# Kernel tuning notes

Hardware: AMD Instinct MI355X
Metric: run time of the kernel (lower is better)

The kernel has to match this reference:

```python
import jax, jax.numpy as jnp
import numpy as np
from jax import lax

B, IMG, P, CIN = 8, 224, 16, 3
D, NH, E, HID, DEPTH, NC = 768, 12, 4, 3072, 12, 1000
NPAT = (IMG // P) ** 2  # 196
S = NPAT + 1            # 197 tokens incl cls
HD = D // NH            # 64
EPS = 1e-5


def _ln(x, g, b):
    m = jnp.mean(x, axis=-1, keepdims=True)
    v = jnp.mean((x - m) ** 2, axis=-1, keepdims=True)
    return (x - m) * lax.rsqrt(v + EPS) * g + b


def setup_inputs() -> dict:
    key = jax.random.key(0)
    ks = list(jax.random.split(key, 24))
    def rn(k, shape, s=0.02):
        return (jax.random.normal(k, shape) * s).astype(jnp.float32)
    inp = {
        "x": jax.random.normal(ks[0], (B, CIN, IMG, IMG), dtype=jnp.float32),
        "patch_w": rn(ks[1], (D, CIN, P, P)),
        "patch_b": jnp.zeros((D,), jnp.float32),
        "cls_token": jnp.zeros((1, 1, D), jnp.float32),
        "pos_embed": rn(ks[2], (1, S, D)),
        "ln1_g": jnp.ones((DEPTH, D), jnp.float32),
        "ln1_b": jnp.zeros((DEPTH, D), jnp.float32),
        "ln2_g": jnp.ones((DEPTH, D), jnp.float32),
        "ln2_b": jnp.zeros((DEPTH, D), jnp.float32),
        "attn_in_w": rn(ks[3], (DEPTH, 3 * D, D)),
        "attn_in_b": jnp.zeros((DEPTH, 3 * D), jnp.float32),
        "attn_out_w": rn(ks[4], (DEPTH, D, D)),
        "attn_out_b": jnp.zeros((DEPTH, D), jnp.float32),
        "gate_w": rn(ks[5], (DEPTH, E, D)),
        "gate_b": jnp.zeros((DEPTH, E), jnp.float32),
        "w1": rn(ks[6], (DEPTH, E, D, HID)),
        "b1": jnp.zeros((DEPTH, E, HID), jnp.float32),
        "w2": rn(ks[7], (DEPTH, E, HID, D)),
        "b2": jnp.zeros((DEPTH, E, D), jnp.float32),
        "head_w": rn(ks[8], (NC, D)),
        "head_b": jnp.zeros((NC,), jnp.float32),
    }
    return inp


def _forward(x, patch_w, patch_b, cls_token, pos_embed, ln1_g, ln1_b, ln2_g, ln2_b,
             attn_in_w, attn_in_b, attn_out_w, attn_out_b, gate_w, gate_b,
             w1, b1, w2, b2, head_w, head_b):
    # Patch embedding: conv stride=patch, then flatten spatial -> tokens
    feat = lax.conv_general_dilated(x, patch_w, window_strides=(P, P), padding="VALID",
                                    dimension_numbers=("NCHW", "OIHW", "NCHW"))
    t = feat.reshape(B, D, NPAT).transpose(0, 2, 1) + patch_b  # [B, 196, D]
    cls = jnp.broadcast_to(cls_token, (B, 1, D))
    h = jnp.concatenate([cls, t], axis=1) + pos_embed  # [B, S, D]

    scale = 1.0 / np.sqrt(HD).astype(np.float32)
    for i in range(DEPTH):
        # ---- attention (query = LN(x); key/value = x, as in source) ----
        qn = _ln(h, ln1_g[i], ln1_b[i])
        wq, wk, wv = attn_in_w[i, :D], attn_in_w[i, D:2 * D], attn_in_w[i, 2 * D:]
        bq, bk, bv = attn_in_b[i, :D], attn_in_b[i, D:2 * D], attn_in_b[i, 2 * D:]
        q = (qn @ wq.T + bq).reshape(B, S, NH, HD)
        k = (h @ wk.T + bk).reshape(B, S, NH, HD)
        v = (h @ wv.T + bv).reshape(B, S, NH, HD)
        scores = jnp.einsum("bqhd,bkhd->bhqk", q, k) * scale
        attn = jax.nn.softmax(scores, axis=-1)
        o = jnp.einsum("bhqk,bkhd->bqhd", attn, v).reshape(B, S, D)
        h = h + o @ attn_out_w[i].T + attn_out_b[i]

        # ---- Top-1 gated MoE MLP ----
        y = _ln(h, ln2_g[i], ln2_b[i])
        logits = y @ gate_w[i].T + gate_b[i]            # [B,S,E]
        probs = jax.nn.softmax(logits, axis=-1)
        top = jnp.argmax(probs, axis=-1)                # [B,S]
        onehot = jax.nn.one_hot(top, E, dtype=y.dtype)  # [B,S,E]
        gv = jnp.sum(probs * onehot, axis=-1)           # [B,S] top-1 gate score
        hidd = jax.nn.gelu(jnp.einsum("bsd,edh->besh", y, w1[i]) + b1[i][None, :, None, :])
        eout = jnp.einsum("besh,ehd->besd", hidd, w2[i]) + b2[i][None, :, None, :]
        moe = jnp.einsum("bse,besd->bsd", onehot, eout) * gv[..., None]
        h = h + moe

    return h[:, 0] @ head_w.T + head_b  # [B, NC]


def reference(x, patch_w, patch_b, cls_token, pos_embed, ln1_g, ln1_b, ln2_g, ln2_b,
              attn_in_w, attn_in_b, attn_out_w, attn_out_b, gate_w, gate_b,
              w1, b1, w2, b2, head_w, head_b):
    return _forward(x, patch_w, patch_b, cls_token, pos_embed, ln1_g, ln1_b, ln2_g,
                    ln2_b, attn_in_w, attn_in_b, attn_out_w, attn_out_b, gate_w,
                    gate_b, w1, b1, w2, b2, head_w, head_b)
```

## Files before the change

### kernel.cpp

```cpp
#include <hip/hip_runtime.h>
#include <math.h>


#define BB 8
#define SS 197
#define DD 768
#define MT (BB*SS)
#define NPATCH 196
#define MPE (BB*NPATCH)
#define HHID 3072
#define NEXP 4
#define QKVN 2304

typedef __bf16 bf16_t;
typedef bf16_t bf16x8 __attribute__((ext_vector_type(8)));
typedef float  f32x4  __attribute__((ext_vector_type(4)));

__device__ __forceinline__ void gload16(const bf16_t* g, bf16_t* l) {
    __builtin_amdgcn_global_load_lds(
        (const __attribute__((address_space(1))) unsigned int*)g,
        (__attribute__((address_space(3))) unsigned int*)l,
        16, 0, 0);
}

__device__ __forceinline__ bf16x8 cvt8(float4 a, float4 b) {
    bf16x8 o;
    o[0]=(bf16_t)a.x; o[1]=(bf16_t)a.y; o[2]=(bf16_t)a.z; o[3]=(bf16_t)a.w;
    o[4]=(bf16_t)b.x; o[5]=(bf16_t)b.y; o[6]=(bf16_t)b.z; o[7]=(bf16_t)b.w;
    return o;
}

__global__ void gather_patches(const float* __restrict__ x, bf16_t* __restrict__ Xp) {
    int i = blockIdx.x * 256 + threadIdx.x;
    if (i >= MPE * DD) return;
    int k = i % DD;
    int m = i / DD;
    int pw = k & 15, ph = (k >> 4) & 15, cin = k >> 8;
    int px = m % 14, py = (m / 14) % 14, b = m / NPATCH;
    int row = py * 16 + ph, col = px * 16 + pw;
    Xp[i] = (bf16_t)x[((size_t)(b * 3 + cin) * 224 + row) * 224 + col];
}

__global__ void build_h(const float* __restrict__ pe, const float* __restrict__ patch_b,
                        const float* __restrict__ cls, const float* __restrict__ pos,
                        float* __restrict__ h) {
    int i = blockIdx.x * 256 + threadIdx.x;
    if (i >= MT * DD) return;
    int d = i % DD;
    int s = (i / DD) % SS;
    int b = i / (DD * SS);
    float v;
    if (s == 0) v = cls[d];
    else        v = pe[((size_t)(b * NPATCH) + (s - 1)) * DD + d] + patch_b[d];
    h[i] = v + pos[s * DD + d];
}

__global__ void cvt_bf16(const float* __restrict__ in, bf16_t* __restrict__ out, int n) {
    int i = (blockIdx.x * 256 + threadIdx.x) * 8;
    if (i >= n) return;
    const float4* p = (const float4*)(in + i);
    *(bf16x8*)(out + i) = cvt8(p[0], p[1]);
}

__global__ __launch_bounds__(256) void transpose_cvt(const float* __restrict__ in,
                                                     bf16_t* __restrict__ out, int R, int C) {
    int z = blockIdx.z;
    in  += (size_t)z * R * C;
    out += (size_t)z * R * C;
    __shared__ float t[32][33];
    int c0 = blockIdx.x * 32, r0 = blockIdx.y * 32;
    int tx = threadIdx.x & 31, ty = threadIdx.x >> 5;
    #pragma unroll
    for (int i = 0; i < 4; i++)
        t[ty + 8*i][tx] = in[(size_t)(r0 + ty + 8*i) * C + c0 + tx];
    __syncthreads();
    #pragma unroll
    for (int i = 0; i < 4; i++)
        out[(size_t)(c0 + ty + 8*i) * R + r0 + tx] = (bf16_t)t[tx][ty + 8*i];
}

template<int BM, int BN, int WM, int WN, int MODE>
__global__ __launch_bounds__((BM/WM)*(BN/WN)*64) void gemm_bf16(
    const bf16_t* __restrict__ A, const bf16_t* __restrict__ A2, int nsplit,
    const bf16_t* __restrict__ Bw,
    const float* __restrict__ bias, float* __restrict__ C, bf16_t* __restrict__ Cb,
    const int* __restrict__ cnt, const int* __restrict__ idx,
    const float* __restrict__ gv, int M, int N, int K)
{
    constexpr int NW  = (BM/WM)*(BN/WN);
    constexpr int WNC = BN/WN;
    constexpr int MI  = WM/16;
    constexpr int NI  = WN/16;
    constexpr int IA  = (BM/8)/NW;
    constexpr int IB  = (BN/8)/NW;
    constexpr bool GATHER = (MODE == 3 || MODE == 4);

    int z = blockIdx.z;
    int count = GATHER ? cnt[z] : M;
    int m0 = blockIdx.y * BM;
    if (m0 >= count) return;
    int n0 = blockIdx.x * BN;
    if (n0 >= nsplit) A = A2;
    Bw += (size_t)z * N * K;
    const float* biasz = bias ? (bias + (size_t)z * N) : nullptr;

    __shared__ bf16_t As[2][BM * 64];
    __shared__ bf16_t Bs[2][BN * 64];
    __shared__ int toks[BM];

    int tid = threadIdx.x, lane = tid & 63, w = tid >> 6;
    if (tid < BM) {
        int mm = m0 + tid;
        if (mm > count - 1) mm = count - 1;
        toks[tid] = GATHER ? idx[z * MT + mm] : mm;
    }
    __syncthreads();

    int wm = (w / WNC) * WM, wn = (w % WNC) * WN;
    int fr = lane & 15, fs = lane >> 4;

    f32x4 acc[MI][NI];
    #pragma unroll
    for (int mi = 0; mi < MI; mi++)
        #pragma unroll
        for (int ni = 0; ni < NI; ni++)
            #pragma unroll
            for (int j = 0; j < 4; j++) acc[mi][ni][j] = 0.f;

    int nk = K >> 6;
    int srow = lane >> 3, scc = lane & 7;

    #define STAGE(buf, k0)                                                              \
        {                                                                               \
            _Pragma("unroll")                                                           \
            for (int i = 0; i < IA; i++) {                                              \
                int blk = i*NW + w;                                                     \
                int row = blk*8 + srow;                                                 \
                const bf16_t* s = A + (size_t)toks[row] * K + (k0) + ((scc ^ (row & 7)) << 3); \
                gload16(s, &As[buf][blk * 512]);                                        \
            }                                                                           \
            _Pragma("unroll")                                                           \
            for (int i = 0; i < IB; i++) {                                              \
                int blk = i*NW + w;                                                     \
                int row = blk*8 + srow;                                                 \
                const bf16_t* s = Bw + (size_t)(n0 + row) * K + (k0) + ((scc ^ (row & 7)) << 3); \
                gload16(s, &Bs[buf][blk * 512]);                                        \
            }                                                                           \
        }

    STAGE(0, 0);
    __syncthreads();
    int cur = 0;
    for (int t = 0; t < nk; t++) {
        if (t + 1 < nk) STAGE(cur ^ 1, (t + 1) << 6);
        #pragma unroll
        for (int ks = 0; ks < 2; ks++) {
            bf16x8 af[MI], bfr[NI];
            #pragma unroll
            for (int mi = 0; mi < MI; mi++) {
                int r = wm + mi * 16 + fr;
                af[mi] = *(bf16x8*)&As[cur][r * 64 + (((fs + ks*4) ^ (r & 7)) << 3)];
            }
            #pragma unroll
            for (int ni = 0; ni < NI; ni++) {
                int r = wn + ni * 16 + fr;
                bfr[ni] = *(bf16x8*)&Bs[cur][r * 64 + (((fs + ks*4) ^ (r & 7)) << 3)];
            }
            #pragma unroll
            for (int mi = 0; mi < MI; mi++)
                #pragma unroll
                for (int ni = 0; ni < NI; ni++)
                    acc[mi][ni] = __builtin_amdgcn_mfma_f32_16x16x32_bf16(af[mi], bfr[ni], acc[mi][ni], 0, 0, 0);
        }
        __syncthreads();
        cur ^= 1;
    }
    #undef STAGE

    #pragma unroll
    for (int mi = 0; mi < MI; mi++) {
        #pragma unroll
        for (int j = 0; j < 4; j++) {
            int rr = wm + mi * 16 + fs * 4 + j;
            if (m0 + rr >= count) continue;
            int crow = toks[rr];
            #pragma unroll
            for (int ni = 0; ni < NI; ni++) {
                int col = n0 + wn + ni * 16 + fr;
                float v = acc[mi][ni][j];
                if (MODE >= 2) v += biasz[col];
                if (MODE == 0) C[(size_t)crow * N + col] = v;
                else if (MODE == 2) C[(size_t)crow * N + col] += v;
                else if (MODE == 3) {
                    float g = 0.5f * v * (1.0f + tanhf(0.7978845608028654f * (v + 0.044715f * v * v * v)));
                    Cb[(size_t)crow * N + col] = (bf16_t)g;
                } else if (MODE == 4) {
                    C[(size_t)crow * N + col] += v * gv[crow];
                } else {
                    Cb[(size_t)crow * N + col] = (bf16_t)v;
                }
            }
        }
    }
}

__global__ __launch_bounds__(256) void ln1_kernel(const float* __restrict__ x,
                                                  const float* __restrict__ g,
                                                  const float* __restrict__ b,
                                                  bf16_t* __restrict__ qn,
                                                  bf16_t* __restrict__ hb)
{
    int m = blockIdx.x, t = threadIdx.x;
    __shared__ float buf[DD];
    __shared__ float tmp[4];
    float s = 0.f;
    for (int j = t; j < DD; j += 256) { float v = x[(size_t)m*DD + j]; buf[j] = v; s += v; }
    #pragma unroll
    for (int o = 32; o > 0; o >>= 1) s += __shfl_down(s, o);
    if ((t & 63) == 0) tmp[t >> 6] = s;
    __syncthreads();
    float mean = (tmp[0]+tmp[1]+tmp[2]+tmp[3]) * (1.0f/DD);
    float s2 = 0.f;
    for (int j = t; j < DD; j += 256) { float d = buf[j] - mean; s2 += d*d; }
    #pragma unroll
    for (int o = 32; o > 0; o >>= 1) s2 += __shfl_down(s2, o);
    __syncthreads();
    if ((t & 63) == 0) tmp[t >> 6] = s2;
    __syncthreads();
    float var = (tmp[0]+tmp[1]+tmp[2]+tmp[3]) * (1.0f/DD);
    float rs = rsqrtf(var + 1e-5f);
    for (int j = t; j < DD; j += 256) {
        qn[(size_t)m*DD + j] = (bf16_t)((buf[j] - mean) * rs * g[j] + b[j]);
        hb[(size_t)m*DD + j] = (bf16_t)buf[j];
    }
}

__global__ __launch_bounds__(256) void ln2_gate_kernel(const float* __restrict__ x,
                                                       const float* __restrict__ g,
                                                       const float* __restrict__ b,
                                                       const float* __restrict__ gw,
                                                       const float* __restrict__ gb,
                                                       bf16_t* __restrict__ yb,
                                                       float* __restrict__ gv,
                                                       int* __restrict__ cnt,
                                                       int* __restrict__ idxb)
{
    int m = blockIdx.x, t = threadIdx.x;
    __shared__ float buf[DD];
    __shared__ float tmp[4];
    __shared__ float red[4][4];
    float s = 0.f;
    for (int j = t; j < DD; j += 256) { float v = x[(size_t)m*DD + j]; buf[j] = v; s += v; }
    #pragma unroll
    for (int o = 32; o > 0; o >>= 1) s += __shfl_down(s, o);
    if ((t & 63) == 0) tmp[t >> 6] = s;
    __syncthreads();
    float mean = (tmp[0]+tmp[1]+tmp[2]+tmp[3]) * (1.0f/DD);
    float s2 = 0.f;
    for (int j = t; j < DD; j += 256) { float d = buf[j] - mean; s2 += d*d; }
    #pragma unroll
    for (int o = 32; o > 0; o >>= 1) s2 += __shfl_down(s2, o);
    __syncthreads();
    if ((t & 63) == 0) tmp[t >> 6] = s2;
    __syncthreads();
    float var = (tmp[0]+tmp[1]+tmp[2]+tmp[3]) * (1.0f/DD);
    float rs = rsqrtf(var + 1e-5f);
    float p0 = 0.f, p1 = 0.f, p2 = 0.f, p3 = 0.f;
    for (int j = t; j < DD; j += 256) {
        float y = (buf[j] - mean) * rs * g[j] + b[j];
        yb[(size_t)m*DD + j] = (bf16_t)y;
        p0 += y * gw[j];
        p1 += y * gw[DD + j];
        p2 += y * gw[2*DD + j];
        p3 += y * gw[3*DD + j];
    }
    #pragma unroll
    for (int o = 32; o > 0; o >>= 1) {
        p0 += __shfl_down(p0, o); p1 += __shfl_down(p1, o);
        p2 += __shfl_down(p2, o); p3 += __shfl_down(p3, o);
    }
    if ((t & 63) == 0) { int ww = t >> 6; red[ww][0]=p0; red[ww][1]=p1; red[ww][2]=p2; red[ww][3]=p3; }
    __syncthreads();
    if (t == 0) {
        float l0 = red[0][0]+red[1][0]+red[2][0]+red[3][0] + gb[0];
        float l1 = red[0][1]+red[1][1]+red[2][1]+red[3][1] + gb[1];
        float l2 = red[0][2]+red[1][2]+red[2][2]+red[3][2] + gb[2];
        float l3 = red[0][3]+red[1][3]+red[2][3]+red[3][3] + gb[3];
        int top = 0; float best = l0;
        if (l1 > best) { best = l1; top = 1; }
        if (l2 > best) { best = l2; top = 2; }
        if (l3 > best) { best = l3; top = 3; }
        float Z = __expf(l0-best) + __expf(l1-best) + __expf(l2-best) + __expf(l3-best);
        gv[m] = 1.0f / Z;
        int pos = atomicAdd(&cnt[top], 1);
        idxb[top * MT + pos] = m;
    }
}

__global__ __launch_bounds__(256) void attn_kernel(const bf16_t* __restrict__ qkv,
                                                   bf16_t* __restrict__ ob)
{
    int qt = blockIdx.x, hh = blockIdx.y, b = blockIdx.z;
    __shared__ bf16_t Qs[64 * 64];
    __shared__ bf16_t Ks[64 * 64];
    __shared__ bf16_t Vt[64 * 72];
    __shared__ float  Sc[64 * 276];
    __shared__ float  linv[64];

    int tid = threadIdx.x, lane = tid & 63, w = tid >> 6;
    int wm = (w >> 1) * 32, wn = (w & 1) * 32;
    int fr = lane & 15, fs = lane >> 4;

    #pragma unroll
    for (int it = 0; it < 2; it++) {
        int row = 8*(it*4 + w) + (lane >> 3), cc = lane & 7;
        int q = qt*64 + row; if (q > SS-1) q = SS-1;
        const bf16_t* src = qkv + ((size_t)(b*SS + q))*QKVN + hh*64 + ((cc ^ (row & 7)) << 3);
        gload16(src, &Qs[(it*4 + w) * 512]);
    }

    for (int kt = 0; kt < 4; kt++) {
        __syncthreads();
        #pragma unroll
        for (int it = 0; it < 2; it++) {
            int row = 8*(it*4 + w) + (lane >> 3), cc = lane & 7;
            int k = kt*64 + row; if (k > SS-1) k = SS-1;
            const bf16_t* src = qkv + ((size_t)(b*SS + k))*QKVN + 768 + hh*64 + ((cc ^ (row & 7)) << 3);
            gload16(src, &Ks[(it*4 + w) * 512]);
        }
        __syncthreads();
        f32x4 acc[2][2];
        #pragma unroll
        for (int mi = 0; mi < 2; mi++)
            #pragma unroll
            for (int ni = 0; ni < 2; ni++)
                #pragma unroll
                for (int j = 0; j < 4; j++) acc[mi][ni][j] = 0.f;
        #pragma unroll
        for (int ks = 0; ks < 2; ks++) {
            bf16x8 af[2], bfr[2];
            #pragma unroll
            for (int mi = 0; mi < 2; mi++) {
                int r = wm + mi * 16 + fr;
                af[mi] = *(bf16x8*)&Qs[r * 64 + (((fs + ks*4) ^ (r & 7)) << 3)];
            }
            #pragma unroll
            for (int ni = 0; ni < 2; ni++) {
                int r = wn + ni * 16 + fr;
                bfr[ni] = *(bf16x8*)&Ks[r * 64 + (((fs + ks*4) ^ (r & 7)) << 3)];
            }
            #pragma unroll
            for (int mi = 0; mi < 2; mi++)
                #pragma unroll
                for (int ni = 0; ni < 2; ni++)
                    acc[mi][ni] = __builtin_amdgcn_mfma_f32_16x16x32_bf16(af[mi], bfr[ni], acc[mi][ni], 0, 0, 0);
        }
        #pragma unroll
        for (int mi = 0; mi < 2; mi++)
            #pragma unroll
            for (int j = 0; j < 4; j++) {
                int qr = wm + mi * 16 + fs * 4 + j;
                #pragma unroll
                for (int ni = 0; ni < 2; ni++) {
                    int col = kt*64 + wn + ni * 16 + fr;
                    float v = acc[mi][ni][j] * 0.125f;
                    if (col > SS-1) v = -1e30f;
                    Sc[qr * 276 + col] = v;
                }
            }
    }
    __syncthreads();

    {
        int row = tid >> 2, c = tid & 3;
        float m = -1e30f;
        for (int i = c; i < 256; i += 4) m = fmaxf(m, Sc[row * 276 + i]);
        m = fmaxf(m, __shfl_xor(m, 1, 4));
        m = fmaxf(m, __shfl_xor(m, 2, 4));
        float s = 0.f;
        for (int i = c; i < 256; i += 4) {
            float e = __expf(Sc[row * 276 + i] - m);
            Sc[row * 276 + i] = e;
            s += e;
        }
        s += __shfl_xor(s, 1, 4);
        s += __shfl_xor(s, 2, 4);
        if (c == 0) linv[row] = 1.0f / s;
    }

    f32x4 pv[2][2];
    #pragma unroll
    for (int mi = 0; mi < 2; mi++)
        #pragma unroll
        for (int ni = 0; ni < 2; ni++)
            #pragma unroll
            for (int j = 0; j < 4; j++) pv[mi][ni][j] = 0.f;

    for (int kt = 0; kt < 4; kt++) {
        __syncthreads();
        {
            int s = tid >> 2, c2 = tid & 3;
            int k = kt*64 + s; if (k > SS-1) k = SS-1;
            const bf16_t* vr = qkv + ((size_t)(b*SS + k))*QKVN + 1536 + hh*64;
            bf16x8 v0 = *(const bf16x8*)(vr + c2*16);
            bf16x8 v1 = *(const bf16x8*)(vr + c2*16 + 8);
            #pragma unroll
            for (int j = 0; j < 8; j++) {
                Vt[(c2*16 + j) * 72 + s]     = v0[j];
                Vt[(c2*16 + 8 + j) * 72 + s] = v1[j];
            }
        }
        __syncthreads();
        #pragma unroll
        for (int ks = 0; ks < 2; ks++) {
            int s0 = kt*64 + ks*32;
            bf16x8 af[2], bfr[2];
            #pragma unroll
            for (int mi = 0; mi < 2; mi++) {
                int qr = wm + mi * 16 + fr;
                const float* p = &Sc[qr * 276 + s0 + fs * 8];
                af[mi] = cvt8(*(const float4*)p, *(const float4*)(p + 4));
            }
            #pragma unroll
            for (int ni = 0; ni < 2; ni++) {
                int d = wn + ni * 16 + fr;
                bfr[ni] = *(bf16x8*)&Vt[d * 72 + ks*32 + fs*8];
            }
            #pragma unroll
            for (int mi = 0; mi < 2; mi++)
                #pragma unroll
                for (int ni = 0; ni < 2; ni++)
                    pv[mi][ni] = __builtin_amdgcn_mfma_f32_16x16x32_bf16(af[mi], bfr[ni], pv[mi][ni], 0, 0, 0);
        }
    }

    #pragma unroll
    for (int mi = 0; mi < 2; mi++)
        #pragma unroll
        for (int j = 0; j < 4; j++) {
            int qr = wm + mi * 16 + fs * 4 + j;
            int q = qt*64 + qr;
            if (q > SS-1) continue;
            float il = linv[qr];
            #pragma unroll
            for (int ni = 0; ni < 2; ni++) {
                int d = wn + ni * 16 + fr;
                ob[((size_t)(b*SS + q))*DD + hh*64 + d] = (bf16_t)(pv[mi][ni][j] * il);
            }
        }
}

__global__ void zero_cnt48(int* cnt) { if (threadIdx.x < 12*NEXP) cnt[threadIdx.x] = 0; }

__global__ void head_kernel(const float* __restrict__ h, const float* __restrict__ hw,
                            const float* __restrict__ hb, float* __restrict__ out)
{
    int i = blockIdx.x * 256 + threadIdx.x;
    if (i >= BB * 1000) return;
    int b = i & 7, n = i >> 3;
    const float4* hr = (const float4*)(h + (size_t)(b * SS) * DD);
    const float4* wr = (const float4*)(hw + (size_t)n * DD);
    float s = 0.f;
    #pragma unroll 4
    for (int k = 0; k < DD/4; k++) {
        float4 a = hr[k], wv = wr[k];
        s += a.x*wv.x + a.y*wv.y + a.z*wv.z + a.w*wv.w;
    }
    out[b * 1000 + n] = s + hb[n];
}

extern "C" void kernel_launch(void* const* d_in, const int* in_sizes, int n_in,
                              void* d_out, int out_size, void* d_ws, size_t ws_size,
                              hipStream_t stream) {
    const float* x          = (const float*)d_in[0];
    const float* patch_w    = (const float*)d_in[1];
    const float* patch_b    = (const float*)d_in[2];
    const float* cls_token  = (const float*)d_in[3];
    const float* pos_embed  = (const float*)d_in[4];
    const float* ln1_g      = (const float*)d_in[5];
    const float* ln1_b      = (const float*)d_in[6];
    const float* ln2_g      = (const float*)d_in[7];
    const float* ln2_b      = (const float*)d_in[8];
    const float* attn_in_w  = (const float*)d_in[9];
    const float* attn_in_b  = (const float*)d_in[10];
    const float* attn_out_w = (const float*)d_in[11];
    const float* attn_out_b = (const float*)d_in[12];
    const float* gate_w     = (const float*)d_in[13];
    const float* gate_b     = (const float*)d_in[14];
    const float* w1         = (const float*)d_in[15];
    const float* b1         = (const float*)d_in[16];
    const float* w2         = (const float*)d_in[17];
    const float* b2         = (const float*)d_in[18];
    const float* head_w     = (const float*)d_in[19];
    const float* head_b     = (const float*)d_in[20];
    float* out = (float*)d_out;

    char* wsb = (char*)d_ws;
    auto alloc = [&](size_t bytes) { char* p = wsb; wsb += (bytes + 63) & ~63ULL; return p; };
    bf16_t* Xp     = (bf16_t*)alloc((size_t)MPE * DD * 2);
    float*  pe     = (float*) alloc((size_t)MPE * DD * 4);
    float*  h      = (float*) alloc((size_t)MT * DD * 4);
    bf16_t* qn_bf  = (bf16_t*)alloc((size_t)MT * DD * 2);
    bf16_t* h_bf   = (bf16_t*)alloc((size_t)MT * DD * 2);
    bf16_t* qkv_bf = (bf16_t*)alloc((size_t)MT * QKVN * 2);
    bf16_t* ob_bf  = (bf16_t*)alloc((size_t)MT * DD * 2);
    bf16_t* yb_bf  = (bf16_t*)alloc((size_t)MT * DD * 2);
    bf16_t* hd_bf  = (bf16_t*)alloc((size_t)MT * HHID * 2);
    float*  gv     = (float*) alloc((size_t)MT * 4);
    int*    cnt    = (int*)   alloc(12 * NEXP * 4);
    int*    idxb   = (int*)   alloc((size_t)12 * NEXP * MT * 4);
    bf16_t* pw_bf  = (bf16_t*)alloc((size_t)DD * DD * 2);
    bf16_t* wq_a   = (bf16_t*)alloc((size_t)12 * QKVN * DD * 2);
    bf16_t* wo_a   = (bf16_t*)alloc((size_t)12 * DD * DD * 2);
    bf16_t* w1t_a  = (bf16_t*)alloc((size_t)12 * NEXP * DD * HHID * 2);
    bf16_t* w2t_a  = (bf16_t*)alloc((size_t)12 * NEXP * DD * HHID * 2);

    dim3 blk(256);
    dim3 blk512(512);
    const int NOSPLIT = 1 << 30;

    zero_cnt48<<<1, 64, 0, stream>>>(cnt);
    cvt_bf16<<<(DD*DD/8 + 255)/256, blk, 0, stream>>>(patch_w, pw_bf, DD*DD);
    cvt_bf16<<<(12*QKVN*DD/8 + 255)/256, blk, 0, stream>>>(attn_in_w, wq_a, 12*QKVN*DD);
    cvt_bf16<<<(12*DD*DD/8 + 255)/256, blk, 0, stream>>>(attn_out_w, wo_a, 12*DD*DD);
    transpose_cvt<<<dim3(HHID/32, DD/32, 12*NEXP), blk, 0, stream>>>(w1, w1t_a, DD, HHID);
    transpose_cvt<<<dim3(DD/32, HHID/32, 12*NEXP), blk, 0, stream>>>(w2, w2t_a, HHID, DD);

    gather_patches<<<(MPE*DD + 255)/256, blk, 0, stream>>>(x, Xp);
    gemm_bf16<64,64,32,32,0><<<dim3(12, 25, 1), blk, 0, stream>>>(
        Xp, nullptr, NOSPLIT, pw_bf, nullptr, pe, nullptr, nullptr, nullptr, nullptr, MPE, DD, DD);
    build_h<<<(MT*DD + 255)/256, blk, 0, stream>>>(pe, patch_b, cls_token, pos_embed, h);

    for (int i = 0; i < 12; i++) {
        const bf16_t* wq_bf = wq_a  + (size_t)i * QKVN * DD;
        const bf16_t* wo_bf = wo_a  + (size_t)i * DD * DD;
        const bf16_t* w1t   = w1t_a + (size_t)i * NEXP * DD * HHID;
        const bf16_t* w2t   = w2t_a + (size_t)i * NEXP * DD * HHID;
        const float* ab    = attn_in_b  + (size_t)i * QKVN;
        const float* obias = attn_out_b + (size_t)i * DD;
        const float* l1g = ln1_g + (size_t)i * DD;
        const float* l1b = ln1_b + (size_t)i * DD;
        const float* l2g = ln2_g + (size_t)i * DD;
        const float* l2b = ln2_b + (size_t)i * DD;
        const float* gw  = gate_w + (size_t)i * NEXP * DD;
        const float* gb  = gate_b + (size_t)i * NEXP;
        const float* b1l = b1 + (size_t)i * NEXP * HHID;
        const float* b2l = b2 + (size_t)i * NEXP * DD;
        int* cnt_i  = cnt  + i * NEXP;
        int* idxb_i = idxb + (size_t)i * NEXP * MT;

        ln1_kernel<<<MT, blk, 0, stream>>>(h, l1g, l1b, qn_bf, h_bf);
        gemm_bf16<128,64,64,32,5><<<dim3(QKVN/64, 13, 1), blk, 0, stream>>>(
            qn_bf, h_bf, DD, wq_bf, ab, nullptr, qkv_bf, nullptr, nullptr, nullptr, MT, QKVN, DD);
        attn_kernel<<<dim3(4, 12, BB), blk, 0, stream>>>(qkv_bf, ob_bf);
        gemm_bf16<64,64,32,32,2><<<dim3(12, 25, 1), blk, 0, stream>>>(
            ob_bf, nullptr, NOSPLIT, wo_bf, obias, h, nullptr, nullptr, nullptr, nullptr, MT, DD, DD);
        ln2_gate_kernel<<<MT, blk, 0, stream>>>(h, l2g, l2b, gw, gb, yb_bf, gv, cnt_i, idxb_i);
        gemm_bf16<128,128,64,32,3><<<dim3(HHID/128, 13, NEXP), blk512, 0, stream>>>(
            yb_bf, nullptr, NOSPLIT, w1t, b1l, nullptr, hd_bf, cnt_i, idxb_i, nullptr, MT, HHID, DD);
        gemm_bf16<128,64,64,32,4><<<dim3(12, 13, NEXP), blk, 0, stream>>>(
            hd_bf, nullptr, NOSPLIT, w2t, b2l, h, nullptr, cnt_i, idxb_i, gv, MT, DD, HHID);
    }

    head_kernel<<<(BB*1000 + 255)/256, blk, 0, stream>>>(h, head_w, head_b, out);
}
```

Baseline: 2.501 ms.

## Use one wave per row for layernorms, fuse bf16 residual copy, shrink attention LDS

LN1 and LN2+gate kernels now give each row one 64-lane wavefront, with float4 loads and xor-shuffle reductions instead of 256-thread blocks that need shared memory and barriers. The bf16 copy of the residual stream moves out of ln1 and is written in build_h and in the MoE down-projection epilogue. The attention kernel shares one LDS buffer for K and transposed V and trims the score row width to 228, so it uses less shared memory and may fit more blocks per CU. The down-projection GEMM switches to 64x64 tiles with more blocks. The epilogue now writes extra bf16 data, and the attention kernel skips PV steps that fall past the sequence length.

```diff
diff --git a/kernel.cpp b/kernel.cpp
--- a/kernel.cpp
+++ b/kernel.cpp
@@ -11,8 +11,10 @@
 #define HHID 3072
 #define NEXP 4
 #define QKVN 2304
+#define SCW 228
 
 typedef __bf16 bf16_t;
+typedef bf16_t bf16x4 __attribute__((ext_vector_type(4)));
 typedef bf16_t bf16x8 __attribute__((ext_vector_type(8)));
 typedef float  f32x4  __attribute__((ext_vector_type(4)));
 
@@ -43,7 +45,7 @@
 
 __global__ void build_h(const float* __restrict__ pe, const float* __restrict__ patch_b,
                         const float* __restrict__ cls, const float* __restrict__ pos,
-                        float* __restrict__ h) {
+                        float* __restrict__ h, bf16_t* __restrict__ hb) {
     int i = blockIdx.x * 256 + threadIdx.x;
     if (i >= MT * DD) return;
     int d = i % DD;
@@ -52,7 +54,9 @@
     float v;
     if (s == 0) v = cls[d];
     else        v = pe[((size_t)(b * NPATCH) + (s - 1)) * DD + d] + patch_b[d];
-    h[i] = v + pos[s * DD + d];
+    float vv = v + pos[s * DD + d];
+    h[i] = vv;
+    hb[i] = (bf16_t)vv;
 }
 
 __global__ void cvt_bf16(const float* __restrict__ in, bf16_t* __restrict__ out, int n) {
@@ -195,7 +199,10 @@
                     float g = 0.5f * v * (1.0f + tanhf(0.7978845608028654f * (v + 0.044715f * v * v * v)));
                     Cb[(size_t)crow * N + col] = (bf16_t)g;
                 } else if (MODE == 4) {
-                    C[(size_t)crow * N + col] += v * gv[crow];
+                    float* p = &C[(size_t)crow * N + col];
+                    float nv = *p + v * gv[crow];
+                    *p = nv;
+                    Cb[(size_t)crow * N + col] = (bf16_t)nv;
                 } else {
                     Cb[(size_t)crow * N + col] = (bf16_t)v;
                 }
@@ -207,31 +214,39 @@
 __global__ __launch_bounds__(256) void ln1_kernel(const float* __restrict__ x,
                                                   const float* __restrict__ g,
                                                   const float* __restrict__ b,
-                                                  bf16_t* __restrict__ qn,
-                                                  bf16_t* __restrict__ hb)
+                                                  bf16_t* __restrict__ qn)
 {
-    int m = blockIdx.x, t = threadIdx.x;
-    __shared__ float buf[DD];
-    __shared__ float tmp[4];
-    float s = 0.f;
-    for (int j = t; j < DD; j += 256) { float v = x[(size_t)m*DD + j]; buf[j] = v; s += v; }
-    #pragma unroll
-    for (int o = 32; o > 0; o >>= 1) s += __shfl_down(s, o);
-    if ((t & 63) == 0) tmp[t >> 6] = s;
-    __syncthreads();
-    float mean = (tmp[0]+tmp[1]+tmp[2]+tmp[3]) * (1.0f/DD);
+    int wid = (blockIdx.x * 256 + threadIdx.x) >> 6;
+    if (wid >= MT) return;
+    int lane = threadIdx.x & 63;
+    const float4* xr = (const float4*)(x + (size_t)wid * DD);
+    float4 v0 = xr[lane], v1 = xr[lane + 64], v2 = xr[lane + 128];
+    float s = v0.x+v0.y+v0.z+v0.w + v1.x+v1.y+v1.z+v1.w + v2.x+v2.y+v2.z+v2.w;
+    #pragma unroll
+    for (int o = 32; o > 0; o >>= 1) s += __shfl_xor(s, o);
+    float mean = s * (1.0f/DD);
     float s2 = 0.f;
-    for (int j = t; j < DD; j += 256) { float d = buf[j] - mean; s2 += d*d; }
-    #pragma unroll
-    for (int o = 32; o > 0; o >>= 1) s2 += __shfl_down(s2, o);
-    __syncthreads();
-    if ((t & 63) == 0) tmp[t >> 6] = s2;
-    __syncthreads();
-    float var = (tmp[0]+tmp[1]+tmp[2]+tmp[3]) * (1.0f/DD);
-    float rs = rsqrtf(var + 1e-5f);
-    for (int j = t; j < DD; j += 256) {
-        qn[(size_t)m*DD + j] = (bf16_t)((buf[j] - mean) * rs * g[j] + b[j]);
-        hb[(size_t)m*DD + j] = (bf16_t)buf[j];
+    #pragma unroll
+    for (int c = 0; c < 3; c++) {
+        float4 v = c == 0 ? v0 : (c == 1 ? v1 : v2);
+        float dx = v.x-mean, dy = v.y-mean, dz = v.z-mean, dw = v.w-mean;
+        s2 += dx*dx + dy*dy + dz*dz + dw*dw;
+    }
+    #pragma unroll
+    for (int o = 32; o > 0; o >>= 1) s2 += __shfl_xor(s2, o);
+    float rs = rsqrtf(s2 * (1.0f/DD) + 1e-5f);
+    const float4* gr = (const float4*)g;
+    const float4* br = (const float4*)b;
+    #pragma unroll
+    for (int c = 0; c < 3; c++) {
+        float4 v = c == 0 ? v0 : (c == 1 ? v1 : v2);
+        float4 gg = gr[lane + 64*c], bb = br[lane + 64*c];
+        bf16x4 o;
+        o[0] = (bf16_t)((v.x - mean) * rs * gg.x + bb.x);
+        o[1] = (bf16_t)((v.y - mean) * rs * gg.y + bb.y);
+        o[2] = (bf16_t)((v.z - mean) * rs * gg.z + bb.z);
+        o[3] = (bf16_t)((v.w - mean) * rs * gg.w + bb.w);
+        *(bf16x4*)(qn + (size_t)wid * DD + (lane + 64*c) * 4) = o;
     }
 }
 
@@ -245,55 +260,63 @@
                                                        int* __restrict__ cnt,
                                                        int* __restrict__ idxb)
 {
-    int m = blockIdx.x, t = threadIdx.x;
-    __shared__ float buf[DD];
-    __shared__ float tmp[4];
-    __shared__ float red[4][4];
-    float s = 0.f;
-    for (int j = t; j < DD; j += 256) { float v = x[(size_t)m*DD + j]; buf[j] = v; s += v; }
-    #pragma unroll
-    for (int o = 32; o > 0; o >>= 1) s += __shfl_down(s, o);
-    if ((t & 63) == 0) tmp[t >> 6] = s;
-    __syncthreads();
-    float mean = (tmp[0]+tmp[1]+tmp[2]+tmp[3]) * (1.0f/DD);
+    int wid = (blockIdx.x * 256 + threadIdx.x) >> 6;
+    if (wid >= MT) return;
+    int lane = threadIdx.x & 63;
+    const float4* xr = (const float4*)(x + (size_t)wid * DD);
+    float4 v0 = xr[lane], v1 = xr[lane + 64], v2 = xr[lane + 128];
+    float s = v0.x+v0.y+v0.z+v0.w + v1.x+v1.y+v1.z+v1.w + v2.x+v2.y+v2.z+v2.w;
+    #pragma unroll
+    for (int o = 32; o > 0; o >>= 1) s += __shfl_xor(s, o);
+    float mean = s * (1.0f/DD);
     float s2 = 0.f;
-    for (int j = t; j < DD; j += 256) { float d = buf[j] - mean; s2 += d*d; }
-    #pragma unroll
-    for (int o = 32; o > 0; o >>= 1) s2 += __shfl_down(s2, o);
-    __syncthreads();
-    if ((t & 63) == 0) tmp[t >> 6] = s2;
-    __syncthreads();
-    float var = (tmp[0]+tmp[1]+tmp[2]+tmp[3]) * (1.0f/DD);
-    float rs = rsqrtf(var + 1e-5f);
+    #pragma unroll
+    for (int c = 0; c < 3; c++) {
+        float4 v = c == 0 ? v0 : (c == 1 ? v1 : v2);
+        float dx = v.x-mean, dy = v.y-mean, dz = v.z-mean, dw = v.w-mean;
+        s2 += dx*dx + dy*dy + dz*dz + dw*dw;
+    }
+    #pragma unroll
+    for (int o = 32; o > 0; o >>= 1) s2 += __shfl_xor(s2, o);
+    float rs = rsqrtf(s2 * (1.0f/DD) + 1e-5f);
+    const float4* gr = (const float4*)g;
+    const float4* br = (const float4*)b;
     float p0 = 0.f, p1 = 0.f, p2 = 0.f, p3 = 0.f;
-    for (int j = t; j < DD; j += 256) {
-        float y = (buf[j] - mean) * rs * g[j] + b[j];
-        yb[(size_t)m*DD + j] = (bf16_t)y;
-        p0 += y * gw[j];
-        p1 += y * gw[DD + j];
-        p2 += y * gw[2*DD + j];
-        p3 += y * gw[3*DD + j];
+    #pragma unroll
+    for (int c = 0; c < 3; c++) {
+        float4 v = c == 0 ? v0 : (c == 1 ? v1 : v2);
+        float4 gg = gr[lane + 64*c], bb = br[lane + 64*c];
+        float y0 = (v.x - mean) * rs * gg.x + bb.x;
+        float y1 = (v.y - mean) * rs * gg.y + bb.y;
+        float y2 = (v.z - mean) * rs * gg.z + bb.z;
+        float y3 = (v.w - mean) * rs * gg.w + bb.w;
+        bf16x4 o; o[0]=(bf16_t)y0; o[1]=(bf16_t)y1; o[2]=(bf16_t)y2; o[3]=(bf16_t)y3;
+        *(bf16x4*)(yb + (size_t)wid * DD + (lane + 64*c) * 4) = o;
+        int off = lane + 64*c;
+        float4 w0 = ((const float4*)(gw          ))[off];
+        float4 w1v = ((const float4*)(gw +   DD  ))[off];
+        float4 w2v = ((const float4*)(gw + 2*DD  ))[off];
+        float4 w3v = ((const float4*)(gw + 3*DD  ))[off];
+        p0 += y0*w0.x + y1*w0.y + y2*w0.z + y3*w0.w;
+        p1 += y0*w1v.x + y1*w1v.y + y2*w1v.z + y3*w1v.w;
+        p2 += y0*w2v.x + y1*w2v.y + y2*w2v.z + y3*w2v.w;
+        p3 += y0*w3v.x + y1*w3v.y + y2*w3v.z + y3*w3v.w;
     }
     #pragma unroll
     for (int o = 32; o > 0; o >>= 1) {
-        p0 += __shfl_down(p0, o); p1 += __shfl_down(p1, o);
-        p2 += __shfl_down(p2, o); p3 += __shfl_down(p3, o);
-    }
-    if ((t & 63) == 0) { int ww = t >> 6; red[ww][0]=p0; red[ww][1]=p1; red[ww][2]=p2; red[ww][3]=p3; }
-    __syncthreads();
-    if (t == 0) {
-        float l0 = red[0][0]+red[1][0]+red[2][0]+red[3][0] + gb[0];
-        float l1 = red[0][1]+red[1][1]+red[2][1]+red[3][1] + gb[1];
-        float l2 = red[0][2]+red[1][2]+red[2][2]+red[3][2] + gb[2];
-        float l3 = red[0][3]+red[1][3]+red[2][3]+red[3][3] + gb[3];
+        p0 += __shfl_xor(p0, o); p1 += __shfl_xor(p1, o);
+        p2 += __shfl_xor(p2, o); p3 += __shfl_xor(p3, o);
+    }
+    if (lane == 0) {
+        float l0 = p0 + gb[0], l1 = p1 + gb[1], l2 = p2 + gb[2], l3 = p3 + gb[3];
         int top = 0; float best = l0;
         if (l1 > best) { best = l1; top = 1; }
         if (l2 > best) { best = l2; top = 2; }
         if (l3 > best) { best = l3; top = 3; }
         float Z = __expf(l0-best) + __expf(l1-best) + __expf(l2-best) + __expf(l3-best);
-        gv[m] = 1.0f / Z;
+        gv[wid] = 1.0f / Z;
         int pos = atomicAdd(&cnt[top], 1);
-        idxb[top * MT + pos] = m;
+        idxb[top * MT + pos] = wid;
     }
 }
 
@@ -302,9 +325,8 @@
 {
     int qt = blockIdx.x, hh = blockIdx.y, b = blockIdx.z;
     __shared__ bf16_t Qs[64 * 64];
-    __shared__ bf16_t Ks[64 * 64];
-    __shared__ bf16_t Vt[64 * 72];
-    __shared__ float  Sc[64 * 276];
+    __shared__ bf16_t KV[64 * 68];
+    __shared__ float  Sc[64 * SCW];
     __shared__ float  linv[64];
 
     int tid = threadIdx.x, lane = tid & 63, w = tid >> 6;
@@ -326,7 +348,7 @@
             int row = 8*(it*4 + w) + (lane >> 3), cc = lane & 7;
             int k = kt*64 + row; if (k > SS-1) k = SS-1;
             const bf16_t* src = qkv + ((size_t)(b*SS + k))*QKVN + 768 + hh*64 + ((cc ^ (row & 7)) << 3);
-            gload16(src, &Ks[(it*4 + w) * 512]);
+            gload16(src, &KV[(it*4 + w) * 512]);
         }
         __syncthreads();
         f32x4 acc[2][2];
@@ -347,7 +369,7 @@
             #pragma unroll
             for (int ni = 0; ni < 2; ni++) {
                 int r = wn + ni * 16 + fr;
-                bfr[ni] = *(bf16x8*)&Ks[r * 64 + (((fs + ks*4) ^ (r & 7)) << 3)];
+                bfr[ni] = *(bf16x8*)&KV[r * 64 + (((fs + ks*4) ^ (r & 7)) << 3)];
             }
             #pragma unroll
             for (int mi = 0; mi < 2; mi++)
@@ -363,9 +385,11 @@
                 #pragma unroll
                 for (int ni = 0; ni < 2; ni++) {
                     int col = kt*64 + wn + ni * 16 + fr;
-                    float v = acc[mi][ni][j] * 0.125f;
-                    if (col > SS-1) v = -1e30f;
-                    Sc[qr * 276 + col] = v;
+                    if (col < SCW) {
+                        float v = acc[mi][ni][j] * 0.125f;
+                        if (col > SS-1) v = -1e30f;
+                        Sc[qr * SCW + col] = v;
+                    }
                 }
             }
     }
@@ -374,13 +398,13 @@
     {
         int row = tid >> 2, c = tid & 3;
         float m = -1e30f;
-        for (int i = c; i < 256; i += 4) m = fmaxf(m, Sc[row * 276 + i]);
+        for (int i = c; i < SCW; i += 4) m = fmaxf(m, Sc[row * SCW + i]);
         m = fmaxf(m, __shfl_xor(m, 1, 4));
         m = fmaxf(m, __shfl_xor(m, 2, 4));
         float s = 0.f;
-        for (int i = c; i < 256; i += 4) {
-            float e = __expf(Sc[row * 276 + i] - m);
-            Sc[row * 276 + i] = e;
+        for (int i = c; i < SCW; i += 4) {
+            float e = __expf(Sc[row * SCW + i] - m);
+            Sc[row * SCW + i] = e;
             s += e;
         }
         s += __shfl_xor(s, 1, 4);
@@ -406,25 +430,26 @@
             bf16x8 v1 = *(const bf16x8*)(vr + c2*16 + 8);
             #pragma unroll
             for (int j = 0; j < 8; j++) {
-                Vt[(c2*16 + j) * 72 + s]     = v0[j];
-                Vt[(c2*16 + 8 + j) * 72 + s] = v1[j];
+                KV[(c2*16 + j) * 68 + s]     = v0[j];
+                KV[(c2*16 + 8 + j) * 68 + s] = v1[j];
             }
         }
         __syncthreads();
         #pragma unroll
         for (int ks = 0; ks < 2; ks++) {
             int s0 = kt*64 + ks*32;
+            if (s0 > SS-1) continue;
             bf16x8 af[2], bfr[2];
             #pragma unroll
             for (int mi = 0; mi < 2; mi++) {
                 int qr = wm + mi * 16 + fr;
-                const float* p = &Sc[qr * 276 + s0 + fs * 8];
+                const float* p = &Sc[qr * SCW + s0 + fs * 8];
                 af[mi] = cvt8(*(const float4*)p, *(const float4*)(p + 4));
             }
             #pragma unroll
             for (int ni = 0; ni < 2; ni++) {
                 int d = wn + ni * 16 + fr;
-                bfr[ni] = *(bf16x8*)&Vt[d * 72 + ks*32 + fs*8];
+                bfr[ni] = *(bf16x8*)&KV[d * 68 + ks*32 + fs*8];
             }
             #pragma unroll
             for (int mi = 0; mi < 2; mi++)
@@ -529,7 +554,7 @@
     gather_patches<<<(MPE*DD + 255)/256, blk, 0, stream>>>(x, Xp);
     gemm_bf16<64,64,32,32,0><<<dim3(12, 25, 1), blk, 0, stream>>>(
         Xp, nullptr, NOSPLIT, pw_bf, nullptr, pe, nullptr, nullptr, nullptr, nullptr, MPE, DD, DD);
-    build_h<<<(MT*DD + 255)/256, blk, 0, stream>>>(pe, patch_b, cls_token, pos_embed, h);
+    build_h<<<(MT*DD + 255)/256, blk, 0, stream>>>(pe, patch_b, cls_token, pos_embed, h, h_bf);
 
     for (int i = 0; i < 12; i++) {
         const bf16_t* wq_bf = wq_a  + (size_t)i * QKVN * DD;
@@ -549,17 +574,18 @@
         int* cnt_i  = cnt  + i * NEXP;
         int* idxb_i = idxb + (size_t)i * NEXP * MT;
 
-        ln1_kernel<<<MT, blk, 0, stream>>>(h, l1g, l1b, qn_bf, h_bf);
+        ln1_kernel<<<dim3((MT*64 + 255)/256), blk, 0, stream>>>(h, l1g, l1b, qn_bf);
         gemm_bf16<128,64,64,32,5><<<dim3(QKVN/64, 13, 1), blk, 0, stream>>>(
             qn_bf, h_bf, DD, wq_bf, ab, nullptr, qkv_bf, nullptr, nullptr, nullptr, MT, QKVN, DD);
         attn_kernel<<<dim3(4, 12, BB), blk, 0, stream>>>(qkv_bf, ob_bf);
         gemm_bf16<64,64,32,32,2><<<dim3(12, 25, 1), blk, 0, stream>>>(
             ob_bf, nullptr, NOSPLIT, wo_bf, obias, h, nullptr, nullptr, nullptr, nullptr, MT, DD, DD);
-        ln2_gate_kernel<<<MT, blk, 0, stream>>>(h, l2g, l2b, gw, gb, yb_bf, gv, cnt_i, idxb_i);
+        ln2_gate_kernel<<<dim3((MT*64 + 255)/256), blk, 0, stream>>>(
+            h, l2g, l2b, gw, gb, yb_bf, gv, cnt_i, idxb_i);
         gemm_bf16<128,128,64,32,3><<<dim3(HHID/128, 13, NEXP), blk512, 0, stream>>>(
             yb_bf, nullptr, NOSPLIT, w1t, b1l, nullptr, hd_bf, cnt_i, idxb_i, nullptr, MT, HHID, DD);
-        gemm_bf16<128,64,64,32,4><<<dim3(12, 13, NEXP), blk, 0, stream>>>(
-            hd_bf, nullptr, NOSPLIT, w2t, b2l, h, nullptr, cnt_i, idxb_i, gv, MT, DD, HHID);
+        gemm_bf16<64,64,32,32,4><<<dim3(12, 25, NEXP), blk, 0, stream>>>(
+            hd_bf, nullptr, NOSPLIT, w2t, b2l, h, h_bf, cnt_i, idxb_i, gv, MT, DD, HHID);
     }
 
     head_kernel<<<(BB*1000 + 255)/256, blk, 0, stream>>>(h, head_w, head_b, out);
```

Result: faster. 2.209 ms (-11.7%).
